# Kernel tuning notes

Measured on AMD Instinct MI355X. Metric: run time of the kernel, lower is better.

The kernel has to match this reference:

```python
import jax, jax.numpy as jnp
import numpy as np

N_NODES = 100000
N_EDGES = 1600000
NODE_DIM = 32
EDGE_DIM = 16
OUT_DIM = 32


def setup_inputs() -> dict:
    key = jax.random.key(0)
    ks = jax.random.split(key, 8)
    D = NODE_DIM + EDGE_DIM  # 48
    return {
        "y": jax.random.normal(ks[0], (N_NODES, NODE_DIM), dtype=jnp.float32),
        "ex": jax.random.normal(ks[1], (N_EDGES, EDGE_DIM), dtype=jnp.float32),
        "W1": jax.random.normal(ks[2], (D, D), dtype=jnp.float32) / np.sqrt(D),
        "b1": jax.random.normal(ks[3], (D,), dtype=jnp.float32) * 0.01,
        "W2": jax.random.normal(ks[4], (OUT_DIM, D), dtype=jnp.float32) / np.sqrt(D),
        "b2": jax.random.normal(ks[5], (OUT_DIM,), dtype=jnp.float32) * 0.01,
        "src": jax.random.randint(ks[6], (N_EDGES,), 0, N_NODES, dtype=jnp.int32),
        "dst": jax.random.randint(ks[7], (N_EDGES,), 0, N_NODES, dtype=jnp.int32),
    }


def reference(y, ex, W1, b1, W2, b2, src, dst):
    n_nodes = y.shape[0]
    # per-edge message: ReLU(Linear(concat(y[src], e_x)))  -> [E, node_dim+edge_dim]
    feat = jnp.concatenate([y[src], ex], axis=1)
    m = jax.nn.relu(feat @ W1.T + b1)
    # mean scatter-reduce onto destination nodes (0 for isolated nodes, DGL semantics)
    s = jax.ops.segment_sum(m, dst, num_segments=n_nodes)
    cnt = jax.ops.segment_sum(jnp.ones((m.shape[0],), m.dtype), dst, num_segments=n_nodes)
    z = jnp.where(cnt[:, None] > 0, s / jnp.maximum(cnt, 1.0)[:, None], 0.0)
    # node update: ReLU(Linear(z)) -> [N, out_dim]
    h = jax.nn.relu(z @ W2.T + b2)
    return h
```

## Files before the change

### kernel.cpp

```cpp
#include <hip/hip_runtime.h>

#define NODE_DIM 32
#define EDGE_DIM 16
#define DD 48
#define OUT_DIM 32
#define MAXDEG 64
#define NXCD 8

typedef _Float16 f16x8 __attribute__((ext_vector_type(8)));
typedef float f32x4 __attribute__((ext_vector_type(4)));

__global__ __launch_bounds__(256)
void prep_kernel(int* __restrict__ cursor, int ZB, int NC,
                 const float* __restrict__ y, _Float16* __restrict__ yh, int N) {
    int b = blockIdx.x;
    if (b < ZB) {
        int i = (b * 256 + threadIdx.x) * 4;
        if (i < NC) *reinterpret_cast<int4*>(cursor + i) = make_int4(0, 0, 0, 0);
        return;
    }
    b -= ZB;
    size_t i = ((size_t)b * 256 + threadIdx.x) * 8;
    if (i < (size_t)N * NODE_DIM) {
        const float4* s0 = reinterpret_cast<const float4*>(y + i);
        const float4 a = s0[0], c = s0[1];
        f16x8 h = {(_Float16)a.x, (_Float16)a.y, (_Float16)a.z, (_Float16)a.w,
                   (_Float16)c.x, (_Float16)c.y, (_Float16)c.z, (_Float16)c.w};
        *reinterpret_cast<f16x8*>(yh + i) = h;
    }
}

__global__ __launch_bounds__(256)
void scatter_kernel(const int* __restrict__ dst, const int* __restrict__ src,
                    int* __restrict__ cursor, int2* __restrict__ meta,
                    int E, int NP) {
    const int xcd = blockIdx.x & (NXCD - 1);
    const int c   = blockIdx.x >> 3;
    const int base = c * 2048 + threadIdx.x * 8;
    if (base >= E) return;

    int dv[8], sv[8];
    if (base + 8 <= E) {
        *reinterpret_cast<int4*>(dv)     = *reinterpret_cast<const int4*>(dst + base);
        *reinterpret_cast<int4*>(dv + 4) = *reinterpret_cast<const int4*>(dst + base + 4);
        *reinterpret_cast<int4*>(sv)     = *reinterpret_cast<const int4*>(src + base);
        *reinterpret_cast<int4*>(sv + 4) = *reinterpret_cast<const int4*>(src + base + 4);
    } else {
#pragma unroll
        for (int i = 0; i < 8; ++i) {
            dv[i] = (base + i < E) ? dst[base + i] : -1;
            sv[i] = (base + i < E) ? src[base + i] : 0;
        }
    }
#pragma unroll
    for (int i = 0; i < 8; ++i) {
        const int d = dv[i];
        if (d >= 0 && (d & (NXCD - 1)) == xcd && base + i < E) {
            int pos = atomicAdd(&cursor[xcd * NP + (d >> 3)], 1);
            if (pos < MAXDEG)
                meta[(size_t)d * MAXDEG + pos] = make_int2(base + i, sv[i]);
        }
    }
}

__global__ __launch_bounds__(256)
void fused_kernel(const _Float16* __restrict__ yh, const float* __restrict__ ex,
                  const float* __restrict__ W1, const float* __restrict__ b1,
                  const float* __restrict__ W2, const float* __restrict__ b2,
                  const int* __restrict__ cursor, const int2* __restrict__ meta,
                  float* __restrict__ out, int N, int NP) {
    __shared__ float w2s[OUT_DIM * 49];
    __shared__ float zb[4][DD];
    __shared__ int2 mlds[4][MAXDEG];

    for (int i = threadIdx.x; i < OUT_DIM * DD; i += 256)
        w2s[(i / DD) * 49 + (i % DD)] = W2[i];
    __syncthreads();

    const int wave = threadIdx.x >> 6;
    const int lane = threadIdx.x & 63;
    const int n = blockIdx.x * 4 + wave;
    const int col = lane & 15;
    const int kg  = lane >> 4;

    f16x8 Blo[3], Bhi[3];
#pragma unroll
    for (int t = 0; t < 3; ++t) {
        const float* wr = W1 + (size_t)(t * 16 + col) * DD;
#pragma unroll
        for (int j = 0; j < 8; ++j) {
            Blo[t][j] = (_Float16)wr[kg * 8 + j];
            Bhi[t][j] = (_Float16)0.f;
        }
        if (kg < 2) {
#pragma unroll
            for (int j = 0; j < 8; ++j)
                Bhi[t][j] = (_Float16)wr[NODE_DIM + kg * 8 + j];
        }
        if (kg == 3) Bhi[t][7] = (_Float16)b1[t * 16 + col];
    }

    const int dg = (n < N) ? cursor[(n & (NXCD - 1)) * NP + (n >> 3)] : 0;
    const int cnt = min(dg, MAXDEG);

    mlds[wave][lane] = (lane < cnt) ? meta[(size_t)n * MAXDEG + lane]
                                    : make_int2(0, 0);

    float pacc0 = 0.f, pacc1 = 0.f, pacc2 = 0.f;
    const int ngroups = (cnt + 15) >> 4;

    for (int g = 0; g < ngroups; ++g) {
        const bool valid = (g * 16 + col) < cnt;
        const int2 md = mlds[wave][g * 16 + col];
        const int eid = md.x, sv = md.y;

        f16x8 alo = *reinterpret_cast<const f16x8*>(
            yh + (size_t)sv * NODE_DIM + kg * 8);

        f16x8 ahi;
#pragma unroll
        for (int j = 0; j < 8; ++j) ahi[j] = (_Float16)0.f;
        if (kg < 2) {
            const float4* ep = reinterpret_cast<const float4*>(
                ex + (size_t)eid * EDGE_DIM + kg * 8);
            const float4 e0 = ep[0], e1 = ep[1];
            ahi[0] = (_Float16)e0.x; ahi[1] = (_Float16)e0.y;
            ahi[2] = (_Float16)e0.z; ahi[3] = (_Float16)e0.w;
            ahi[4] = (_Float16)e1.x; ahi[5] = (_Float16)e1.y;
            ahi[6] = (_Float16)e1.z; ahi[7] = (_Float16)e1.w;
        }
        if (kg == 3) ahi[7] = (_Float16)1.f;

        if (!valid) {
#pragma unroll
            for (int j = 0; j < 8; ++j) { alo[j] = (_Float16)0.f; ahi[j] = (_Float16)0.f; }
        }

#pragma unroll
        for (int t = 0; t < 3; ++t) {
            f32x4 c = {0.f, 0.f, 0.f, 0.f};
            c = __builtin_amdgcn_mfma_f32_16x16x32_f16(alo, Blo[t], c, 0, 0, 0);
            c = __builtin_amdgcn_mfma_f32_16x16x32_f16(ahi, Bhi[t], c, 0, 0, 0);
#pragma unroll
            for (int r = 0; r < 4; ++r) {
                const float v = fmaxf(c[r], 0.f);
                if (t == 0) pacc0 += v;
                else if (t == 1) pacc1 += v;
                else pacc2 += v;
            }
        }
    }

    pacc0 += __shfl_xor(pacc0, 16); pacc0 += __shfl_xor(pacc0, 32);
    pacc1 += __shfl_xor(pacc1, 16); pacc1 += __shfl_xor(pacc1, 32);
    pacc2 += __shfl_xor(pacc2, 16); pacc2 += __shfl_xor(pacc2, 32);

    if (n < N && lane < 16) {
        const float inv = (dg > 0) ? 1.f / (float)dg : 0.f;
        zb[wave][lane]      = pacc0 * inv;
        zb[wave][lane + 16] = pacc1 * inv;
        zb[wave][lane + 32] = pacc2 * inv;
    }
    __syncthreads();

    if (n < N && lane < OUT_DIM) {
        float a = b2[lane];
#pragma unroll
        for (int k = 0; k < DD; ++k)
            a = fmaf(zb[wave][k], w2s[lane * 49 + k], a);
        out[(size_t)n * OUT_DIM + lane] = fmaxf(a, 0.f);
    }
}

extern "C" void kernel_launch(void* const* d_in, const int* in_sizes, int n_in,
                              void* d_out, int out_size, void* d_ws, size_t ws_size,
                              hipStream_t stream) {
    const float* y  = (const float*)d_in[0];
    const float* ex = (const float*)d_in[1];
    const float* W1 = (const float*)d_in[2];
    const float* b1 = (const float*)d_in[3];
    const float* W2 = (const float*)d_in[4];
    const float* b2 = (const float*)d_in[5];
    const int* src  = (const int*)d_in[6];
    const int* dst  = (const int*)d_in[7];

    const int N = in_sizes[0] / NODE_DIM;
    const int E = in_sizes[6];
    const int NP = (N + NXCD - 1) / NXCD;
    const int NC = ((NXCD * NP + 3) / 4) * 4;

    int* cursor = (int*)d_ws;
    size_t off  = ((size_t)NC * sizeof(int) + 255) & ~(size_t)255;
    int2* meta  = (int2*)((char*)d_ws + off);
    _Float16* yh = (_Float16*)((char*)meta + (size_t)N * MAXDEG * sizeof(int2));

    const int ZB  = (NC / 4 + 255) / 256;
    const int CBy = (N * NODE_DIM / 8 + 255) / 256;

    prep_kernel<<<ZB + CBy, 256, 0, stream>>>(cursor, ZB, NC, y, yh, N);

    const int K = (E + 2047) / 2048;
    scatter_kernel<<<K * NXCD, 256, 0, stream>>>(dst, src, cursor, meta, E, NP);

    const int NB = (N + 3) / 4;
    fused_kernel<<<NB, 256, 0, stream>>>(yh, ex, W1, b1, W2, b2,
                                         cursor, meta, (float*)d_out, N, NP);
}
```

Before: 211.2 us.

## Pre-sort edge features into destination-bucketed fp16 buffer during scatter

The scatter kernel now reads each edge's 16-float feature row and writes it as fp16 into a per-destination slot buffer next to a separate source-index buffer. The fused kernel then reads edge features contiguously per node instead of gathering fp32 rows by edge id. This trades the random fp32 gather in the fused kernel for extra reads and scattered fp16 writes in the scatter kernel. The bucketed feature buffer (N*64*16 halfs) also adds a large workspace footprint and write traffic for slots that are mostly empty.

```diff
diff --git a/kernel.cpp b/kernel.cpp
--- a/kernel.cpp
+++ b/kernel.cpp
@@ -32,8 +32,9 @@
 
 __global__ __launch_bounds__(256)
 void scatter_kernel(const int* __restrict__ dst, const int* __restrict__ src,
-                    int* __restrict__ cursor, int2* __restrict__ meta,
-                    int E, int NP) {
+                    const float* __restrict__ ex,
+                    int* __restrict__ cursor, int* __restrict__ srcbuf,
+                    _Float16* __restrict__ exbuf, int E, int NP) {
     const int xcd = blockIdx.x & (NXCD - 1);
     const int c   = blockIdx.x >> 3;
     const int base = c * 2048 + threadIdx.x * 8;
@@ -57,21 +58,33 @@
         const int d = dv[i];
         if (d >= 0 && (d & (NXCD - 1)) == xcd && base + i < E) {
             int pos = atomicAdd(&cursor[xcd * NP + (d >> 3)], 1);
-            if (pos < MAXDEG)
-                meta[(size_t)d * MAXDEG + pos] = make_int2(base + i, sv[i]);
+            if (pos < MAXDEG) {
+                const size_t slot = (size_t)d * MAXDEG + pos;
+                srcbuf[slot] = sv[i];
+                const float4* ep = reinterpret_cast<const float4*>(
+                    ex + (size_t)(base + i) * EDGE_DIM);
+                const float4 a = ep[0], b = ep[1], cc = ep[2], dd = ep[3];
+                f16x8 h0 = {(_Float16)a.x, (_Float16)a.y, (_Float16)a.z, (_Float16)a.w,
+                            (_Float16)b.x, (_Float16)b.y, (_Float16)b.z, (_Float16)b.w};
+                f16x8 h1 = {(_Float16)cc.x, (_Float16)cc.y, (_Float16)cc.z, (_Float16)cc.w,
+                            (_Float16)dd.x, (_Float16)dd.y, (_Float16)dd.z, (_Float16)dd.w};
+                f16x8* outp = reinterpret_cast<f16x8*>(exbuf + slot * EDGE_DIM);
+                outp[0] = h0;
+                outp[1] = h1;
+            }
         }
     }
 }
 
 __global__ __launch_bounds__(256)
-void fused_kernel(const _Float16* __restrict__ yh, const float* __restrict__ ex,
+void fused_kernel(const _Float16* __restrict__ yh, const _Float16* __restrict__ exbuf,
                   const float* __restrict__ W1, const float* __restrict__ b1,
                   const float* __restrict__ W2, const float* __restrict__ b2,
-                  const int* __restrict__ cursor, const int2* __restrict__ meta,
+                  const int* __restrict__ cursor, const int* __restrict__ srcbuf,
                   float* __restrict__ out, int N, int NP) {
     __shared__ float w2s[OUT_DIM * 49];
     __shared__ float zb[4][DD];
-    __shared__ int2 mlds[4][MAXDEG];
+    __shared__ int srcb[4][MAXDEG];
 
     for (int i = threadIdx.x; i < OUT_DIM * DD; i += 256)
         w2s[(i / DD) * 49 + (i % DD)] = W2[i];
@@ -103,33 +116,29 @@
     const int dg = (n < N) ? cursor[(n & (NXCD - 1)) * NP + (n >> 3)] : 0;
     const int cnt = min(dg, MAXDEG);
 
-    mlds[wave][lane] = (lane < cnt) ? meta[(size_t)n * MAXDEG + lane]
-                                    : make_int2(0, 0);
+    srcb[wave][lane] = (lane < cnt) ? srcbuf[(size_t)n * MAXDEG + lane] : 0;
+
+    const _Float16* exb = exbuf + (size_t)n * MAXDEG * EDGE_DIM;
 
     float pacc0 = 0.f, pacc1 = 0.f, pacc2 = 0.f;
     const int ngroups = (cnt + 15) >> 4;
 
     for (int g = 0; g < ngroups; ++g) {
-        const bool valid = (g * 16 + col) < cnt;
-        const int2 md = mlds[wave][g * 16 + col];
-        const int eid = md.x, sv = md.y;
+        const int row = g * 16 + col;
+        const bool valid = row < cnt;
+        const int sv = srcb[wave][row];
 
         f16x8 alo = *reinterpret_cast<const f16x8*>(
             yh + (size_t)sv * NODE_DIM + kg * 8);
 
         f16x8 ahi;
-#pragma unroll
-        for (int j = 0; j < 8; ++j) ahi[j] = (_Float16)0.f;
         if (kg < 2) {
-            const float4* ep = reinterpret_cast<const float4*>(
-                ex + (size_t)eid * EDGE_DIM + kg * 8);
-            const float4 e0 = ep[0], e1 = ep[1];
-            ahi[0] = (_Float16)e0.x; ahi[1] = (_Float16)e0.y;
-            ahi[2] = (_Float16)e0.z; ahi[3] = (_Float16)e0.w;
-            ahi[4] = (_Float16)e1.x; ahi[5] = (_Float16)e1.y;
-            ahi[6] = (_Float16)e1.z; ahi[7] = (_Float16)e1.w;
-        }
-        if (kg == 3) ahi[7] = (_Float16)1.f;
+            ahi = *reinterpret_cast<const f16x8*>(exb + (size_t)row * EDGE_DIM + kg * 8);
+        } else {
+#pragma unroll
+            for (int j = 0; j < 8; ++j) ahi[j] = (_Float16)0.f;
+            if (kg == 3) ahi[7] = (_Float16)1.f;
+        }
 
         if (!valid) {
 #pragma unroll
@@ -191,8 +200,11 @@
 
     int* cursor = (int*)d_ws;
     size_t off  = ((size_t)NC * sizeof(int) + 255) & ~(size_t)255;
-    int2* meta  = (int2*)((char*)d_ws + off);
-    _Float16* yh = (_Float16*)((char*)meta + (size_t)N * MAXDEG * sizeof(int2));
+    int* srcbuf = (int*)((char*)d_ws + off);
+    _Float16* exbuf = (_Float16*)((char*)srcbuf +
+                      (size_t)N * MAXDEG * sizeof(int));
+    _Float16* yh = (_Float16*)((char*)exbuf +
+                   (size_t)N * MAXDEG * EDGE_DIM * sizeof(_Float16));
 
     const int ZB  = (NC / 4 + 255) / 256;
     const int CBy = (N * NODE_DIM / 8 + 255) / 256;
@@ -200,9 +212,10 @@
     prep_kernel<<<ZB + CBy, 256, 0, stream>>>(cursor, ZB, NC, y, yh, N);
 
     const int K = (E + 2047) / 2048;
-    scatter_kernel<<<K * NXCD, 256, 0, stream>>>(dst, src, cursor, meta, E, NP);
+    scatter_kernel<<<K * NXCD, 256, 0, stream>>>(dst, src, ex, cursor,
+                                                 srcbuf, exbuf, E, NP);
 
     const int NB = (N + 3) / 4;
-    fused_kernel<<<NB, 256, 0, stream>>>(yh, ex, W1, b1, W2, b2,
-                                         cursor, meta, (float*)d_out, N, NP);
-}
+    fused_kernel<<<NB, 256, 0, stream>>>(yh, exbuf, W1, b1, W2, b2,
+                                         cursor, srcbuf, (float*)d_out, N, NP);
+}
```

New measurement: 266.5 us. 1.26x slower.
